# Kernel optimization log

Measured on AMD Instinct MI355X. Metric: run time of the kernel, lower is better.

The kernel has to match this reference:

```python
import jax, jax.numpy as jnp
import numpy as np

BSZ, SEQ, DIM, NH = 2, 2048, 2048, 16
HD = DIM // NH  # 128


def setup_inputs() -> dict:
    key = jax.random.key(0)
    ks = jax.random.split(key, 6)
    x = jax.random.normal(ks[0], (BSZ, SEQ, DIM), dtype=jnp.float32)
    # torch Linear weights: [out_features, in_features]
    scale = 1.0 / np.sqrt(DIM)
    wq = jax.random.normal(ks[1], (DIM, DIM), dtype=jnp.float32) * scale
    wk = jax.random.normal(ks[2], (DIM, DIM), dtype=jnp.float32) * scale
    wv = jax.random.normal(ks[3], (DIM, DIM), dtype=jnp.float32) * scale
    wo = jax.random.normal(ks[4], (DIM, DIM), dtype=jnp.float32) * scale
    # RoPE freqs (llama style): theta=10000
    inv_freq = 1.0 / (10000.0 ** (jnp.arange(0, HD, 2, dtype=jnp.float32) / HD))  # [HD//2]
    t = jnp.arange(SEQ, dtype=jnp.float32)
    angles = jnp.outer(t, inv_freq)  # [SEQ, HD//2]
    freqs_cos = jnp.cos(angles)
    freqs_sin = jnp.sin(angles)
    # causal additive mask [SEQ, SEQ]
    mask = jnp.where(jnp.tril(jnp.ones((SEQ, SEQ), dtype=bool)), 0.0, -jnp.inf).astype(jnp.float32)
    return {"x": x, "wq": wq, "wk": wk, "wv": wv, "wo": wo,
            "freqs_cos": freqs_cos, "freqs_sin": freqs_sin, "mask": mask}


def _apply_rope(v, cos, sin):
    # v: [b, s, h, hd]; complex pairs are interleaved (even=real, odd=imag)
    b, s, h, hd = v.shape
    vr = v.reshape(b, s, h, hd // 2, 2)
    v0, v1 = vr[..., 0], vr[..., 1]
    c = cos[None, :, None, :]  # [1, s, 1, hd//2]
    sn = sin[None, :, None, :]
    out = jnp.stack([v0 * c - v1 * sn, v0 * sn + v1 * c], axis=-1)
    return out.reshape(b, s, h, hd)


def reference(x, wq, wk, wv, wo, freqs_cos, freqs_sin, mask):
    b, s, _ = x.shape
    xq = (x @ wq.T).reshape(b, s, NH, HD)
    xk = (x @ wk.T).reshape(b, s, NH, HD)
    xv = (x @ wv.T).reshape(b, s, NH, HD)
    xq = _apply_rope(xq, freqs_cos, freqs_sin)
    xk = _apply_rope(xk, freqs_cos, freqs_sin)
    # [b, h, s, s]
    scores = jnp.einsum('bqhd,bkhd->bhqk', xq, xk) / jnp.sqrt(jnp.float32(HD))
    scores = scores + mask[None, None, :, :]
    probs = jax.nn.softmax(scores.astype(jnp.float32), axis=-1).astype(scores.dtype)
    out = jnp.einsum('bhqk,bkhd->bqhd', probs, xv).reshape(b, s, NH * HD)
    return out @ wo.T
```

## Files before the change

### kernel.cpp

```cpp
#include <hip/hip_runtime.h>
#include <hip/hip_bf16.h>
#include <stdint.h>

typedef __bf16 bf16x8 __attribute__((ext_vector_type(8)));
typedef float f32x4 __attribute__((ext_vector_type(4)));
typedef unsigned short u16;
typedef unsigned int u32;

#define DEVI __device__ __forceinline__

DEVI u16 f2b(float f){ __bf16 h = (__bf16)f; return __builtin_bit_cast(u16, h); }
DEVI float b2f(u16 u){ return (float)__builtin_bit_cast(__bf16, u); }

constexpr int BSZ = 2, SEQ = 2048, DIM = 2048, NH = 16, HD = 128;

#if defined(__has_builtin)
#if __has_builtin(__builtin_amdgcn_global_load_lds)
#define HAVE_ASYNC_LDS 1
#endif
#endif

DEVI void cp16(void* lds, const void* g){
#ifdef HAVE_ASYNC_LDS
  auto gp = (const __attribute__((address_space(1))) u32*)(uintptr_t)g;
  auto lp = (__attribute__((address_space(3))) u32*)(uintptr_t)lds;
  __builtin_amdgcn_global_load_lds(gp, lp, 16, 0, 0);
#else
  *(uint4*)lds = *(const uint4*)g;
#endif
}

__global__ __launch_bounds__(256) void k_convert(
    const float* __restrict__ x, const float* __restrict__ wq,
    const float* __restrict__ wk, const float* __restrict__ wv,
    const float* __restrict__ wo,
    u16* __restrict__ xb, u16* __restrict__ wqkv, u16* __restrict__ wob)
{
  int e = (blockIdx.x * 256 + threadIdx.x) * 4;
  float4 v; u16* dp;
  if (e < 8388608){
    v = *(const float4*)&x[e]; dp = &xb[e];
  } else if (e < 20971520){
    int o = e - 8388608; int sec = o >> 22; int oo = o & 4194303;
    const float* w = (sec == 0) ? wq : ((sec == 1) ? wk : wv);
    v = *(const float4*)&w[oo]; dp = &wqkv[o];
  } else {
    int o = e - 20971520;
    v = *(const float4*)&wo[o]; dp = &wob[o];
  }
  ushort4 r; r.x = f2b(v.x); r.y = f2b(v.y); r.z = f2b(v.z); r.w = f2b(v.w);
  *(ushort4*)dp = r;
}

__global__ __launch_bounds__(256) void k_gemm_qkv(
    const u16* __restrict__ A, const u16* __restrict__ W,
    const float* __restrict__ fc, const float* __restrict__ fs,
    u16* __restrict__ Qd, u16* __restrict__ Kd, u16* __restrict__ Vt)
{
  __shared__ u16 smem[128*136];
  u16* As = smem;
  u16* Bs = smem + 4096;
  u16* Cs = smem;
  const int t = threadIdx.x;
  const int lane = t & 63;
  const int l15 = lane & 15, quad = lane >> 4;
  const int wave = t >> 6;
  const int wr = (wave >> 1) * 64, wc = (wave & 1) * 64;
  const int tm = blockIdx.y * 128, tn = blockIdx.x * 128;
  const int arow = t >> 2, acol = (t & 3) * 8;
  const int sec = tn >> 11;
  const int hh = (tn & 2047) >> 7;
  const int bb = tm >> 11, s0 = tm & 2047;

  f32x4 acc[4][4] = {};
  for (int k0 = 0; k0 < DIM; k0 += 32){
    __syncthreads();
    #pragma unroll
    for (int is = 0; is < 2; ++is){
      int row = is*64 + arow;
      cp16(&As[is*2048 + t*8], &A[(size_t)(tm + row)*DIM + k0 + acol]);
      cp16(&Bs[is*2048 + t*8], &W[(size_t)(tn + row)*DIM + k0 + acol]);
    }
    __syncthreads();
    bf16x8 af[4], bfr[4];
    #pragma unroll
    for (int i = 0; i < 4; ++i){
      af[i]  = *(const bf16x8*)&As[(wr + i*16 + l15)*32 + quad*8];
      bfr[i] = *(const bf16x8*)&Bs[(wc + i*16 + l15)*32 + quad*8];
    }
    #pragma unroll
    for (int mt = 0; mt < 4; ++mt)
      #pragma unroll
      for (int nt = 0; nt < 4; ++nt)
        acc[mt][nt] = __builtin_amdgcn_mfma_f32_16x16x32_bf16(af[mt], bfr[nt], acc[mt][nt], 0, 0, 0);
  }
  __syncthreads();
  if (sec < 2){
    #pragma unroll
    for (int mt = 0; mt < 4; ++mt)
      #pragma unroll
      for (int nt = 0; nt < 4; ++nt)
        #pragma unroll
        for (int r = 0; r < 4; ++r)
          Cs[(wr + mt*16 + quad*4 + r)*136 + wc + nt*16 + l15] = f2b(acc[mt][nt][r]);
  } else {
    #pragma unroll
    for (int mt = 0; mt < 4; ++mt)
      #pragma unroll
      for (int nt = 0; nt < 4; ++nt)
        #pragma unroll
        for (int r = 0; r < 4; ++r)
          Cs[(wc + nt*16 + l15)*136 + wr + mt*16 + quad*4 + r] = f2b(acc[mt][nt][r]);
  }
  __syncthreads();

  const float qs = (sec == 0) ? (0.08838834764831845f * 1.4426950408889634f) : 1.0f;
  const int col0 = (t & 15) * 8;
  if (sec < 2){
    u16* dst = (sec == 0) ? Qd : Kd;
    #pragma unroll
    for (int jj = 0; jj < 8; ++jj){
      int row = (t >> 4) + jj*16;
      int s = s0 + row;
      uint4 cv = *(const uint4*)&Cs[row*136 + col0];
      const u16* cp = (const u16*)&cv;
      u16 op[8];
      float4 c4 = *(const float4*)&fc[(size_t)s*64 + (col0 >> 1)];
      float4 s4 = *(const float4*)&fs[(size_t)s*64 + (col0 >> 1)];
      float cc[4] = {c4.x*qs, c4.y*qs, c4.z*qs, c4.w*qs};
      float ss[4] = {s4.x*qs, s4.y*qs, s4.z*qs, s4.w*qs};
      #pragma unroll
      for (int p = 0; p < 4; ++p){
        float a = b2f(cp[2*p]), bv = b2f(cp[2*p+1]);
        op[2*p]   = f2b(a*cc[p] - bv*ss[p]);
        op[2*p+1] = f2b(a*ss[p] + bv*cc[p]);
      }
      *(uint4*)&dst[((size_t)(bb*NH + hh)*SEQ + s)*HD + col0] = *(const uint4*)op;
    }
  } else {
    const size_t vbase = ((size_t)(bb*NH + hh))*HD*SEQ;
    #pragma unroll
    for (int jj = 0; jj < 8; ++jj){
      int d = (t >> 4) + jj*16;
      uint4 cv = *(const uint4*)&Cs[d*136 + col0];
      *(uint4*)&Vt[vbase + (size_t)d*SEQ + s0 + col0] = cv;
    }
  }
}

__global__ __launch_bounds__(512) void k_flash(
    const u16* __restrict__ Qd, const u16* __restrict__ Kd,
    const u16* __restrict__ Vt, u16* __restrict__ OP0, u16* __restrict__ OP1,
    float* __restrict__ Mp, float* __restrict__ Lp)
{
  __shared__ u16 Ks[64*136];
  __shared__ u16 Vs[128*72];
  __shared__ u16 Ps[8*16*72];

  const int t = threadIdx.x, lane = t & 63, wave = t >> 6;
  const int l15 = lane & 15, quad = lane >> 4;
  const int j = blockIdx.x >> 1, split = blockIdx.x & 1;
  const int h = blockIdx.y, b = blockIdx.z, bh = b*NH + h;
  const size_t base  = (size_t)bh * SEQ * HD;
  const size_t baseT = (size_t)bh * HD * SEQ;
  u16* Psw = &Ps[wave*16*72];
  u16* OPs = split ? OP1 : OP0;
  const int lo = 17*split, hi = lo + 17;
  const int qt0 = j, qt1 = 15 - j;
  const int len0 = 2*qt0 + 2;

  const int krow = t >> 4, kcol = (t & 15) * 8;
  const int vrow = t >> 3, vcol = (t & 7) * 8;

  for (int pass = 0; pass < 2; ++pass){
    const int qt = pass ? qt1 : qt0;
    const int len = 2*qt + 2;
    int kt0 = pass ? (lo - len0) : lo; if (kt0 < 0) kt0 = 0;
    int kt1 = pass ? (hi - len0) : hi; if (kt1 > len) kt1 = len;
    const int qb = qt*128 + wave*16;

    bf16x8 qf[4];
    #pragma unroll
    for (int ks = 0; ks < 4; ++ks)
      qf[ks] = *(const bf16x8*)&Qd[base + (size_t)(qb + l15)*HD + ks*32 + quad*8];

    f32x4 oacc[8] = {};
    float m_s = -1e30f, l_s = 0.f;

    if (kt0 < kt1){
      uint4 kreg[2], vreg[2];
      #pragma unroll
      for (int i = 0; i < 2; ++i){
        kreg[i] = *(const uint4*)&Kd[base + (size_t)(kt0*64 + i*32 + krow)*HD + kcol];
        vreg[i] = *(const uint4*)&Vt[baseT + (size_t)(i*64 + vrow)*SEQ + kt0*64 + vcol];
      }
      for (int kt = kt0; kt < kt1; ++kt){
        __syncthreads();
        #pragma unroll
        for (int i = 0; i < 2; ++i){
          *(uint4*)&Ks[(i*32 + krow)*136 + kcol] = kreg[i];
          *(uint4*)&Vs[(i*64 + vrow)*72 + vcol] = vreg[i];
        }
        __syncthreads();
        if (kt + 1 < kt1){
          #pragma unroll
          for (int i = 0; i < 2; ++i){
            kreg[i] = *(const uint4*)&Kd[base + (size_t)((kt+1)*64 + i*32 + krow)*HD + kcol];
            vreg[i] = *(const uint4*)&Vt[baseT + (size_t)(i*64 + vrow)*SEQ + (kt+1)*64 + vcol];
          }
        }
        if (kt*64 <= qb + 15){
          f32x4 sacc[4] = {};
          #pragma unroll
          for (int ks = 0; ks < 4; ++ks){
            bf16x8 kf[4];
            #pragma unroll
            for (int nk = 0; nk < 4; ++nk)
              kf[nk] = *(const bf16x8*)&Ks[(nk*16 + l15)*136 + ks*32 + quad*8];
            #pragma unroll
            for (int nk = 0; nk < 4; ++nk)
              sacc[nk] = __builtin_amdgcn_mfma_f32_16x16x32_bf16(kf[nk], qf[ks], sacc[nk], 0, 0, 0);
          }
          if (kt*64 + 63 > qb){
            int q = qb + l15;
            #pragma unroll
            for (int nk = 0; nk < 4; ++nk)
              #pragma unroll
              for (int r = 0; r < 4; ++r){
                int key = kt*64 + nk*16 + quad*4 + r;
                if (key > q) sacc[nk][r] = -1e30f;
              }
          }
          float m4[4];
          #pragma unroll
          for (int nk = 0; nk < 4; ++nk)
            m4[nk] = fmaxf(fmaxf(sacc[nk][0], sacc[nk][1]), fmaxf(sacc[nk][2], sacc[nk][3]));
          float rm = fmaxf(fmaxf(m4[0], m4[1]), fmaxf(m4[2], m4[3]));
          rm = fmaxf(rm, __shfl_xor(rm, 16));
          rm = fmaxf(rm, __shfl_xor(rm, 32));
          float mnew = fmaxf(m_s, rm);
          float alpha = exp2f(m_s - mnew);
          m_s = mnew;
          float s4[4];
          #pragma unroll
          for (int nk = 0; nk < 4; ++nk){
            u16 pk[4];
            float p0 = exp2f(sacc[nk][0] - mnew);
            float p1 = exp2f(sacc[nk][1] - mnew);
            float p2 = exp2f(sacc[nk][2] - mnew);
            float p3 = exp2f(sacc[nk][3] - mnew);
            pk[0] = f2b(p0); pk[1] = f2b(p1); pk[2] = f2b(p2); pk[3] = f2b(p3);
            s4[nk] = (p0 + p1) + (p2 + p3);
            *(uint2*)&Psw[l15*72 + nk*16 + quad*4] = *(const uint2*)pk;
          }
          float rs = (s4[0] + s4[1]) + (s4[2] + s4[3]);
          rs += __shfl_xor(rs, 16);
          rs += __shfl_xor(rs, 32);
          l_s = l_s*alpha + rs;
          #pragma unroll
          for (int db = 0; db < 8; ++db)
            #pragma unroll
            for (int r = 0; r < 4; ++r) oacc[db][r] *= alpha;
          #pragma unroll
          for (int k2 = 0; k2 < 2; ++k2){
            bf16x8 pf = *(const bf16x8*)&Psw[l15*72 + k2*32 + quad*8];
            #pragma unroll
            for (int db = 0; db < 8; ++db){
              bf16x8 vf = *(const bf16x8*)&Vs[(db*16 + l15)*72 + k2*32 + quad*8];
              oacc[db] = __builtin_amdgcn_mfma_f32_16x16x32_bf16(vf, pf, oacc[db], 0, 0, 0);
            }
          }
        }
      }
    }
    {
      int s = qb + l15;
      #pragma unroll
      for (int db = 0; db < 8; ++db){
        u16 ok[4];
        #pragma unroll
        for (int r = 0; r < 4; ++r) ok[r] = f2b(oacc[db][r]);
        *(uint2*)&OPs[(((size_t)(b*SEQ + s))*NH + h)*HD + db*16 + quad*4] = *(const uint2*)ok;
      }
      if (quad == 0){
        size_t mi = ((size_t)split*BSZ*NH + bh)*SEQ + s;
        Mp[mi] = m_s;
        Lp[mi] = l_s;
      }
    }
  }
}

__global__ __launch_bounds__(256) void k_combine(
    u16* __restrict__ OP0, const u16* __restrict__ OP1,
    const float* __restrict__ Mp, const float* __restrict__ Lp)
{
  size_t flat = ((size_t)blockIdx.x*256 + threadIdx.x)*8;
  int h = (int)((flat >> 7) & 15);
  int s = (int)((flat >> 11) & 2047);
  int b = (int)(flat >> 22);
  size_t row = ((size_t)(b*NH + h))*SEQ + s;
  const size_t off1 = (size_t)BSZ*NH*SEQ;
  float m0 = Mp[row], l0 = Lp[row];
  float m1 = Mp[row + off1], l1 = Lp[row + off1];
  float m = fmaxf(m0, m1);
  float w0 = exp2f(m0 - m), w1 = exp2f(m1 - m);
  float inv = 1.0f / (w0*l0 + w1*l1);
  uint4 a = *(const uint4*)&OP0[flat];
  uint4 c = *(const uint4*)&OP1[flat];
  const u16* pa = (const u16*)&a;
  const u16* pc = (const u16*)&c;
  u16 o[8];
  #pragma unroll
  for (int i = 0; i < 8; ++i)
    o[i] = f2b((b2f(pa[i])*w0 + b2f(pc[i])*w1) * inv);
  *(uint4*)&OP0[flat] = *(const uint4*)o;
}

__global__ __launch_bounds__(256) void k_gemm_out(
    const u16* __restrict__ A, const u16* __restrict__ W, float* __restrict__ out)
{
  __shared__ u16 As[128*32];
  __shared__ u16 Bs[128*32];
  const int t = threadIdx.x;
  const int lane = t & 63;
  const int l15 = lane & 15, quad = lane >> 4;
  const int wave = t >> 6;
  const int wr = (wave >> 1) * 64, wc = (wave & 1) * 64;
  const int tm = blockIdx.y * 128, tn = blockIdx.x * 128;
  const int arow = t >> 2, acol = (t & 3) * 8;

  f32x4 acc[4][4] = {};
  for (int k0 = 0; k0 < DIM; k0 += 32){
    __syncthreads();
    #pragma unroll
    for (int is = 0; is < 2; ++is){
      int row = is*64 + arow;
      cp16(&As[is*2048 + t*8], &A[(size_t)(tm + row)*DIM + k0 + acol]);
      cp16(&Bs[is*2048 + t*8], &W[(size_t)(tn + row)*DIM + k0 + acol]);
    }
    __syncthreads();
    bf16x8 af[4], bfr[4];
    #pragma unroll
    for (int i = 0; i < 4; ++i){
      af[i]  = *(const bf16x8*)&As[(wr + i*16 + l15)*32 + quad*8];
      bfr[i] = *(const bf16x8*)&Bs[(wc + i*16 + l15)*32 + quad*8];
    }
    #pragma unroll
    for (int mt = 0; mt < 4; ++mt)
      #pragma unroll
      for (int nt = 0; nt < 4; ++nt)
        acc[mt][nt] = __builtin_amdgcn_mfma_f32_16x16x32_bf16(af[mt], bfr[nt], acc[mt][nt], 0, 0, 0);
  }
  #pragma unroll
  for (int mt = 0; mt < 4; ++mt)
    #pragma unroll
    for (int nt = 0; nt < 4; ++nt)
      #pragma unroll
      for (int r = 0; r < 4; ++r){
        int row = tm + wr + mt*16 + quad*4 + r;
        int col = tn + wc + nt*16 + l15;
        out[(size_t)row*DIM + col] = acc[mt][nt][r];
      }
}

extern "C" void kernel_launch(void* const* d_in, const int* in_sizes, int n_in,
                              void* d_out, int out_size, void* d_ws, size_t ws_size,
                              hipStream_t stream)
{
  const float* x  = (const float*)d_in[0];
  const float* wq = (const float*)d_in[1];
  const float* wk = (const float*)d_in[2];
  const float* wv = (const float*)d_in[3];
  const float* wo = (const float*)d_in[4];
  const float* fc = (const float*)d_in[5];
  const float* fs = (const float*)d_in[6];
  float* out = (float*)d_out;

  char* ws = (char*)d_ws;
  u16* xb   = (u16*)(ws);
  u16* wqkv = (u16*)(ws + 16777216);
  u16* wob  = (u16*)(ws + 41943040);
  u16* Qr   = (u16*)(ws + 50331648);
  u16* Kr   = (u16*)(ws + 67108864);
  u16* Vt   = (u16*)(ws + 83886080);
  u16* Ob   = (u16*)(ws + 100663296);
  u16* OP1  = wqkv;
  float* Mp = (float*)(ws + 33554432);
  float* Lp = (float*)(ws + 34078720);

  k_convert <<<24576, 256, 0, stream>>>(x, wq, wk, wv, wo, xb, wqkv, wob);
  k_gemm_qkv<<<dim3(48, 32), 256, 0, stream>>>(xb, wqkv, fc, fs, Qr, Kr, Vt);
  k_flash   <<<dim3(16, NH, BSZ), 512, 0, stream>>>(Qr, Kr, Vt, Ob, OP1, Mp, Lp);
  k_combine <<<4096, 256, 0, stream>>>(Ob, OP1, Mp, Lp);
  k_gemm_out<<<dim3(16, 32), 256, 0, stream>>>(Ob, wob, out);
}
```

Before: 458.0 us.

## Load K/V fragments directly from global memory, dropping LDS staging and block barriers

```diff
diff --git a/kernel.cpp b/kernel.cpp
--- a/kernel.cpp
+++ b/kernel.cpp
@@ -153,8 +153,6 @@
     const u16* __restrict__ Vt, u16* __restrict__ OP0, u16* __restrict__ OP1,
     float* __restrict__ Mp, float* __restrict__ Lp)
 {
-  __shared__ u16 Ks[64*136];
-  __shared__ u16 Vs[128*72];
   __shared__ u16 Ps[8*16*72];
 
   const int t = threadIdx.x, lane = t & 63, wave = t >> 6;
@@ -169,15 +167,13 @@
   const int qt0 = j, qt1 = 15 - j;
   const int len0 = 2*qt0 + 2;
 
-  const int krow = t >> 4, kcol = (t & 15) * 8;
-  const int vrow = t >> 3, vcol = (t & 7) * 8;
-
   for (int pass = 0; pass < 2; ++pass){
     const int qt = pass ? qt1 : qt0;
     const int len = 2*qt + 2;
     int kt0 = pass ? (lo - len0) : lo; if (kt0 < 0) kt0 = 0;
     int kt1 = pass ? (hi - len0) : hi; if (kt1 > len) kt1 = len;
     const int qb = qt*128 + wave*16;
+    int kend = (qb >> 6) + 1; if (kend > kt1) kend = kt1;
 
     bf16x8 qf[4];
     #pragma unroll
@@ -187,89 +183,76 @@
     f32x4 oacc[8] = {};
     float m_s = -1e30f, l_s = 0.f;
 
-    if (kt0 < kt1){
-      uint4 kreg[2], vreg[2];
-      #pragma unroll
-      for (int i = 0; i < 2; ++i){
-        kreg[i] = *(const uint4*)&Kd[base + (size_t)(kt0*64 + i*32 + krow)*HD + kcol];
-        vreg[i] = *(const uint4*)&Vt[baseT + (size_t)(i*64 + vrow)*SEQ + kt0*64 + vcol];
-      }
-      for (int kt = kt0; kt < kt1; ++kt){
-        __syncthreads();
-        #pragma unroll
-        for (int i = 0; i < 2; ++i){
-          *(uint4*)&Ks[(i*32 + krow)*136 + kcol] = kreg[i];
-          *(uint4*)&Vs[(i*64 + vrow)*72 + vcol] = vreg[i];
-        }
-        __syncthreads();
-        if (kt + 1 < kt1){
-          #pragma unroll
-          for (int i = 0; i < 2; ++i){
-            kreg[i] = *(const uint4*)&Kd[base + (size_t)((kt+1)*64 + i*32 + krow)*HD + kcol];
-            vreg[i] = *(const uint4*)&Vt[baseT + (size_t)(i*64 + vrow)*SEQ + (kt+1)*64 + vcol];
-          }
-        }
-        if (kt*64 <= qb + 15){
-          f32x4 sacc[4] = {};
-          #pragma unroll
-          for (int ks = 0; ks < 4; ++ks){
-            bf16x8 kf[4];
-            #pragma unroll
-            for (int nk = 0; nk < 4; ++nk)
-              kf[nk] = *(const bf16x8*)&Ks[(nk*16 + l15)*136 + ks*32 + quad*8];
-            #pragma unroll
-            for (int nk = 0; nk < 4; ++nk)
-              sacc[nk] = __builtin_amdgcn_mfma_f32_16x16x32_bf16(kf[nk], qf[ks], sacc[nk], 0, 0, 0);
-          }
-          if (kt*64 + 63 > qb){
-            int q = qb + l15;
-            #pragma unroll
-            for (int nk = 0; nk < 4; ++nk)
-              #pragma unroll
-              for (int r = 0; r < 4; ++r){
-                int key = kt*64 + nk*16 + quad*4 + r;
-                if (key > q) sacc[nk][r] = -1e30f;
-              }
-          }
-          float m4[4];
+    for (int kt = kt0; kt < kend; ++kt){
+      const u16* kp = &Kd[base + (size_t)(kt*64)*HD];
+      f32x4 sacc[4] = {};
+      bf16x8 kf[4];
+      #pragma unroll
+      for (int nk = 0; nk < 4; ++nk)
+        kf[nk] = *(const bf16x8*)&kp[(size_t)(nk*16 + l15)*HD + quad*8];
+      #pragma unroll
+      for (int ks = 0; ks < 4; ++ks){
+        bf16x8 kn[4];
+        if (ks < 3){
           #pragma unroll
           for (int nk = 0; nk < 4; ++nk)
-            m4[nk] = fmaxf(fmaxf(sacc[nk][0], sacc[nk][1]), fmaxf(sacc[nk][2], sacc[nk][3]));
-          float rm = fmaxf(fmaxf(m4[0], m4[1]), fmaxf(m4[2], m4[3]));
-          rm = fmaxf(rm, __shfl_xor(rm, 16));
-          rm = fmaxf(rm, __shfl_xor(rm, 32));
-          float mnew = fmaxf(m_s, rm);
-          float alpha = exp2f(m_s - mnew);
-          m_s = mnew;
-          float s4[4];
+            kn[nk] = *(const bf16x8*)&kp[(size_t)(nk*16 + l15)*HD + (ks+1)*32 + quad*8];
+        }
+        #pragma unroll
+        for (int nk = 0; nk < 4; ++nk)
+          sacc[nk] = __builtin_amdgcn_mfma_f32_16x16x32_bf16(kf[nk], qf[ks], sacc[nk], 0, 0, 0);
+        if (ks < 3){
           #pragma unroll
-          for (int nk = 0; nk < 4; ++nk){
-            u16 pk[4];
-            float p0 = exp2f(sacc[nk][0] - mnew);
-            float p1 = exp2f(sacc[nk][1] - mnew);
-            float p2 = exp2f(sacc[nk][2] - mnew);
-            float p3 = exp2f(sacc[nk][3] - mnew);
-            pk[0] = f2b(p0); pk[1] = f2b(p1); pk[2] = f2b(p2); pk[3] = f2b(p3);
-            s4[nk] = (p0 + p1) + (p2 + p3);
-            *(uint2*)&Psw[l15*72 + nk*16 + quad*4] = *(const uint2*)pk;
+          for (int nk = 0; nk < 4; ++nk) kf[nk] = kn[nk];
+        }
+      }
+      if (kt == (qb >> 6)){
+        int q = qb + l15;
+        #pragma unroll
+        for (int nk = 0; nk < 4; ++nk)
+          #pragma unroll
+          for (int r = 0; r < 4; ++r){
+            int key = kt*64 + nk*16 + quad*4 + r;
+            if (key > q) sacc[nk][r] = -1e30f;
           }
-          float rs = (s4[0] + s4[1]) + (s4[2] + s4[3]);
-          rs += __shfl_xor(rs, 16);
-          rs += __shfl_xor(rs, 32);
-          l_s = l_s*alpha + rs;
-          #pragma unroll
-          for (int db = 0; db < 8; ++db)
-            #pragma unroll
-            for (int r = 0; r < 4; ++r) oacc[db][r] *= alpha;
-          #pragma unroll
-          for (int k2 = 0; k2 < 2; ++k2){
-            bf16x8 pf = *(const bf16x8*)&Psw[l15*72 + k2*32 + quad*8];
-            #pragma unroll
-            for (int db = 0; db < 8; ++db){
-              bf16x8 vf = *(const bf16x8*)&Vs[(db*16 + l15)*72 + k2*32 + quad*8];
-              oacc[db] = __builtin_amdgcn_mfma_f32_16x16x32_bf16(vf, pf, oacc[db], 0, 0, 0);
-            }
-          }
+      }
+      float m4[4];
+      #pragma unroll
+      for (int nk = 0; nk < 4; ++nk)
+        m4[nk] = fmaxf(fmaxf(sacc[nk][0], sacc[nk][1]), fmaxf(sacc[nk][2], sacc[nk][3]));
+      float rm = fmaxf(fmaxf(m4[0], m4[1]), fmaxf(m4[2], m4[3]));
+      rm = fmaxf(rm, __shfl_xor(rm, 16));
+      rm = fmaxf(rm, __shfl_xor(rm, 32));
+      float mnew = fmaxf(m_s, rm);
+      float alpha = exp2f(m_s - mnew);
+      m_s = mnew;
+      float s4[4];
+      #pragma unroll
+      for (int nk = 0; nk < 4; ++nk){
+        u16 pk[4];
+        float p0 = exp2f(sacc[nk][0] - mnew);
+        float p1 = exp2f(sacc[nk][1] - mnew);
+        float p2 = exp2f(sacc[nk][2] - mnew);
+        float p3 = exp2f(sacc[nk][3] - mnew);
+        pk[0] = f2b(p0); pk[1] = f2b(p1); pk[2] = f2b(p2); pk[3] = f2b(p3);
+        s4[nk] = (p0 + p1) + (p2 + p3);
+        *(uint2*)&Psw[l15*72 + nk*16 + quad*4] = *(const uint2*)pk;
+      }
+      float rs = (s4[0] + s4[1]) + (s4[2] + s4[3]);
+      rs += __shfl_xor(rs, 16);
+      rs += __shfl_xor(rs, 32);
+      l_s = l_s*alpha + rs;
+      #pragma unroll
+      for (int db = 0; db < 8; ++db)
+        #pragma unroll
+        for (int r = 0; r < 4; ++r) oacc[db][r] *= alpha;
+      #pragma unroll
+      for (int k2 = 0; k2 < 2; ++k2){
+        bf16x8 pf = *(const bf16x8*)&Psw[l15*72 + k2*32 + quad*8];
+        #pragma unroll
+        for (int db = 0; db < 8; ++db){
+          bf16x8 vf = *(const bf16x8*)&Vt[baseT + (size_t)(db*16 + l15)*SEQ + kt*64 + k2*32 + quad*8];
+          oacc[db] = __builtin_amdgcn_mfma_f32_16x16x32_bf16(vf, pf, oacc[db], 0, 0, 0);
         }
       }
     }
```

New measurement: 566.4 us. +23.7%, slower.
